# Kernel optimization log

Measured on AMD Instinct MI355X. Metric: run time of the kernel, lower is better.

The kernel has to match this reference:

```python
import jax, jax.numpy as jnp
import numpy as np

D_MODEL = 1024
NHEAD = 16
HEAD_DIM = D_MODEL // NHEAD
SF_THRESHOLD = 4.0
SF_LEVELS = 8
STEP = SF_THRESHOLD / SF_LEVELS  # quantization step of ScaleAndFireNeuron
EPS = 1e-6


def setup_inputs() -> dict:
    key = jax.random.key(0)
    ks = jax.random.split(key, 12)
    B, L, D = 2, 2048, D_MODEL
    s = 1.0 / np.sqrt(D)
    inp = {
        "x": jax.random.normal(ks[0], (B, L, D), dtype=jnp.float32),
        "wq": jax.random.normal(ks[1], (D, D), dtype=jnp.float32) * s,
        "bq": jnp.zeros((D,), dtype=jnp.float32),
        "wk": jax.random.normal(ks[2], (D, D), dtype=jnp.float32) * s,
        "bk": jnp.zeros((D,), dtype=jnp.float32),
        "wv": jax.random.normal(ks[3], (D, D), dtype=jnp.float32) * s,
        "bv": jnp.zeros((D,), dtype=jnp.float32),
        "wo": jax.random.normal(ks[4], (D, D), dtype=jnp.float32) * s,
        "bo": jnp.zeros((D,), dtype=jnp.float32),
        "gq": jnp.ones((HEAD_DIM,), dtype=jnp.float32),  # SpikingQKNorm gain (q)
        "gk": jnp.ones((HEAD_DIM,), dtype=jnp.float32),  # SpikingQKNorm gain (k)
    }
    return inp


def _rms_norm(t, g):
    # SpikingQKNorm: RMS normalization over head_dim with learned gain
    return t * jax.lax.rsqrt(jnp.mean(t * t, axis=-1, keepdims=True) + EPS) * g


def _sfn(t):
    # ScaleAndFireNeuron: T=1 multi-level spike quantization with straight-through estimator.
    # Levels are integer multiples of STEP, clipped to +/- SF_LEVELS.
    q = jnp.clip(jnp.round(t / STEP), -SF_LEVELS, SF_LEVELS) * STEP
    return t + jax.lax.stop_gradient(q - t)


def reference(x, wq, bq, wk, bk, wv, bv, wo, bo, gq, gk):
    B, L, D = x.shape
    H, Dh = NHEAD, HEAD_DIM
    scale = Dh ** -0.5

    def proj(w, b):
        return (x @ w.T + b).reshape(B, L, H, Dh).transpose(0, 2, 1, 3)  # [B,H,L,Dh]

    q = _sfn(_rms_norm(proj(wq, bq), gq))
    k = _sfn(_rms_norm(proj(wk, bk), gk))
    v = _sfn(proj(wv, bv))

    scores = jnp.einsum('bhqd,bhkd->bhqk', q, k) * scale  # [B,H,L,L]
    probs = jax.nn.softmax(scores, axis=-1)
    out = jnp.einsum('bhqk,bhkd->bhqd', probs, v)  # [B,H,L,Dh]
    out = out.transpose(0, 2, 1, 3).reshape(B, L, D)
    return out @ wo.T + bo
```

## Files before the change

### kernel.cpp

```cpp
#include <hip/hip_runtime.h>
#include <stdint.h>

#define D_MODEL 1024
#define NHEAD 16
#define HEAD_DIM 64
#define SEQ 2048
#define BATCH 2
#define MROWS (BATCH*SEQ)
#define KVBLK 128
#define KVTILES (SEQ/KVBLK)

typedef unsigned short u16;
typedef short bf16x8 __attribute__((ext_vector_type(8)));
typedef float f32x4 __attribute__((ext_vector_type(4)));
typedef float f32x16 __attribute__((ext_vector_type(16)));

__device__ inline float bf2f(u16 h){ return __uint_as_float(((unsigned)h)<<16); }
__device__ inline u16 f2bf(float x){
  unsigned u = __float_as_uint(x);
  unsigned r = (u + 0x7FFFu + ((u>>16)&1u)) >> 16;
  return (u16)r;
}

__device__ inline f32x4 mfma_bf16(bf16x8 a, bf16x8 b, f32x4 c){
  return __builtin_amdgcn_mfma_f32_16x16x32_bf16(a, b, c, 0, 0, 0);
}
__device__ inline f32x16 mfma32_bf16(bf16x8 a, bf16x8 b, f32x16 c){
  return __builtin_amdgcn_mfma_f32_32x32x16_bf16(a, b, c, 0, 0, 0);
}

__device__ inline void gld_lds16(const u16* g, u16* l){
  __builtin_amdgcn_global_load_lds(
      (const __attribute__((address_space(1))) void*)g,
      (__attribute__((address_space(3))) void*)l, 16, 0, 0);
}

__device__ inline int swz8(int row){ return (row ^ (row >> 3)) & 7; }

__device__ inline uint32_t pack_bf2(float p0, float p1){
  uint32_t u0 = __float_as_uint(p0) + 0x8000u;
  uint32_t u1 = __float_as_uint(p1) + 0x8000u;
  return __builtin_amdgcn_perm(u1, u0, 0x07060302u);
}

__global__ __launch_bounds__(256) void pack_split(const float* __restrict__ src,
                                                  u16* __restrict__ hi, u16* __restrict__ lo, int n4){
  int i = blockIdx.x*256 + threadIdx.x;
  if (i >= n4) return;
  float4 v = ((const float4*)src)[i];
  float vv[4] = {v.x, v.y, v.z, v.w};
  u16 h[4], l[4];
  #pragma unroll
  for (int j=0;j<4;j++){
    h[j] = f2bf(vv[j]);
    l[j] = f2bf(vv[j] - bf2f(h[j]));
  }
  ((ushort4*)hi)[i] = make_ushort4(h[0],h[1],h[2],h[3]);
  ((ushort4*)lo)[i] = make_ushort4(l[0],l[1],l[2],l[3]);
}

__global__ __launch_bounds__(256) void pack_w(const float* __restrict__ wq, const float* __restrict__ wk,
                                              const float* __restrict__ wv, const float* __restrict__ wo,
                                              u16* __restrict__ qkv_hi, u16* __restrict__ qkv_lo,
                                              u16* __restrict__ wo_hi, u16* __restrict__ wo_lo){
  int which = blockIdx.x >> 10;
  int i = ((blockIdx.x & 1023) << 8) + threadIdx.x;
  const float* src = which==0 ? wq : which==1 ? wk : which==2 ? wv : wo;
  u16* hi = (which==3) ? wo_hi : qkv_hi + ((size_t)which << 20);
  u16* lo = (which==3) ? wo_lo : qkv_lo + ((size_t)which << 20);
  float4 v = ((const float4*)src)[i];
  float vv[4] = {v.x, v.y, v.z, v.w};
  u16 h[4], l[4];
  #pragma unroll
  for (int j=0;j<4;j++){
    h[j] = f2bf(vv[j]);
    l[j] = f2bf(vv[j] - bf2f(h[j]));
  }
  ((ushort4*)hi)[i] = make_ushort4(h[0],h[1],h[2],h[3]);
  ((ushort4*)lo)[i] = make_ushort4(l[0],l[1],l[2],l[3]);
}

__global__ __launch_bounds__(256) void pack_bias(const float* __restrict__ bq, const float* __restrict__ bk,
                                                 const float* __restrict__ bv, float* __restrict__ out){
  int i = blockIdx.x*256 + threadIdx.x;
  if (i < 1024) out[i] = bq[i];
  else if (i < 2048) out[i] = bk[i-1024];
  else if (i < 3072) out[i] = bv[i-2048];
}

__global__ __launch_bounds__(256) void gemm_qkv(
    const u16* __restrict__ a_hi, const u16* __restrict__ a_lo,
    const u16* __restrict__ b_hi, const u16* __restrict__ b_lo,
    const float* __restrict__ bias,
    u16* __restrict__ qb, u16* __restrict__ kb, u16* __restrict__ vb,
    const float* __restrict__ gq, const float* __restrict__ gk)
{
  __shared__ u16 lds[2][12288];
  const int tid = threadIdx.x;
  const int lane = tid & 63;
  const int w = tid >> 6;
  const int wr = w >> 1, wc = w & 1;
  const int m0 = blockIdx.x * 128;
  const int n0 = blockIdx.y * 128;
  const int K = 1024;

  f32x4 acc[4][4];
  #pragma unroll
  for (int i=0;i<4;i++)
    #pragma unroll
    for (int j=0;j<4;j++) acc[i][j] = (f32x4){0.f,0.f,0.f,0.f};

  auto stage = [&](int buf, int kt){
    u16* base = &lds[buf][0];
    if (kt < 32){
      int kk = kt << 5;
      #pragma unroll
      for (int r=0;r<2;r++){
        const u16* g = a_hi + (size_t)(m0 + (tid>>2) + r*64)*K + kk + (tid&3)*8;
        gld_lds16(g, base + w*512 + r*2048);
      }
      #pragma unroll
      for (int r=0;r<2;r++){
        const u16* g = a_lo + (size_t)(m0 + (tid>>2) + r*64)*K + kk + (tid&3)*8;
        gld_lds16(g, base + 4096 + w*512 + r*2048);
      }
      #pragma unroll
      for (int r=0;r<2;r++){
        const u16* g = b_hi + (size_t)(n0 + (tid>>2) + r*64)*K + kk + (tid&3)*8;
        gld_lds16(g, base + 8192 + w*512 + r*2048);
      }
    } else {
      int kk = (kt-32) << 5;
      #pragma unroll
      for (int r=0;r<2;r++){
        const u16* g = a_hi + (size_t)(m0 + (tid>>2) + r*64)*K + kk + (tid&3)*8;
        gld_lds16(g, base + w*512 + r*2048);
      }
      #pragma unroll
      for (int r=0;r<2;r++){
        const u16* g = b_lo + (size_t)(n0 + (tid>>2) + r*64)*K + kk + (tid&3)*8;
        gld_lds16(g, base + 8192 + w*512 + r*2048);
      }
    }
  };

  const int koff = (lane>>4)*8;
  const int rowa = wr*64 + (lane&15);
  const int rowb = wc*64 + (lane&15);

  stage(0, 0);
  for (int kt=0; kt<64; ++kt){
    __syncthreads();
    if (kt+1 < 64) stage((kt+1)&1, kt+1);
    const u16* la = &lds[kt&1][0];
    const u16* lb = &lds[kt&1][8192];
    bf16x8 bfv[4];
    #pragma unroll
    for (int j=0;j<4;j++) bfv[j] = *(const bf16x8*)&lb[(rowb + j*16)*32 + koff];
    bf16x8 af[4];
    #pragma unroll
    for (int i=0;i<4;i++) af[i] = *(const bf16x8*)&la[(rowa + i*16)*32 + koff];
    #pragma unroll
    for (int i=0;i<4;i++)
      #pragma unroll
      for (int j=0;j<4;j++)
        acc[i][j] = mfma_bf16(af[i], bfv[j], acc[i][j]);
    if (kt < 32){
      const u16* ll = &lds[kt&1][4096];
      bf16x8 al[4];
      #pragma unroll
      for (int i=0;i<4;i++) al[i] = *(const bf16x8*)&ll[(rowa + i*16)*32 + koff];
      #pragma unroll
      for (int i=0;i<4;i++)
        #pragma unroll
        for (int j=0;j<4;j++)
          acc[i][j] = mfma_bf16(al[i], bfv[j], acc[i][j]);
    }
  }

  const int gcolbase = n0 + wc*64;
  const int sidx = gcolbase >> 6;
  const int ttype = sidx < 16 ? 0 : (sidx < 32 ? 1 : 2);
  u16* dst = ttype==0 ? qb : (ttype==1 ? kb : vb);
  const int h = sidx - (ttype==1 ? 16 : (ttype==2 ? 32 : 0));
  float gvals[4], bvals[4];
  #pragma unroll
  for (int j=0;j<4;j++){
    int dh = j*16 + (lane&15);
    bvals[j] = bias[gcolbase + dh];
    gvals[j] = ttype==0 ? gq[dh] : (ttype==1 ? gk[dh] : 1.0f);
  }
  #pragma unroll
  for (int i=0;i<4;i++){
    #pragma unroll
    for (int r=0;r<4;r++){
      float tv[4];
      float ssq = 0.f;
      #pragma unroll
      for (int j=0;j<4;j++){ tv[j] = acc[i][j][r] + bvals[j]; ssq += tv[j]*tv[j]; }
      ssq += __shfl_xor(ssq, 1);
      ssq += __shfl_xor(ssq, 2);
      ssq += __shfl_xor(ssq, 4);
      ssq += __shfl_xor(ssq, 8);
      float s = 1.0f;
      if (ttype < 2) s = 1.0f / sqrtf(ssq * (1.0f/64.0f) + 1e-6f);
      int row = m0 + wr*64 + i*16 + (lane>>4)*4 + r;
      int bi = row >> 11, li = row & 2047;
      size_t obase = ((size_t)(bi*NHEAD + h)*SEQ + li)*HEAD_DIM;
      #pragma unroll
      for (int j=0;j<4;j++){
        float val = tv[j] * s * gvals[j];
        float z = rintf(val * 2.0f);
        z = fminf(8.0f, fmaxf(-8.0f, z));
        dst[obase + j*16 + (lane&15)] = f2bf(z * 0.5f);
      }
    }
  }
}

__global__ __launch_bounds__(256) void gemm_bt(
    const u16* __restrict__ a_hi, const u16* __restrict__ b_hi,
    const float* __restrict__ bias, float* __restrict__ out_f,
    int M, int N, int K)
{
  __shared__ u16 lds[2][8192];
  const int tid = threadIdx.x;
  const int lane = tid & 63;
  const int w = tid >> 6;
  const int wr = w >> 1, wc = w & 1;
  const int m0 = blockIdx.x * 128;
  const int n0 = blockIdx.y * 128;
  const int NT = K / 32;

  f32x4 acc[4][4];
  #pragma unroll
  for (int i=0;i<4;i++)
    #pragma unroll
    for (int j=0;j<4;j++) acc[i][j] = (f32x4){0.f,0.f,0.f,0.f};

  auto stage = [&](int buf, int kt){
    int kk = kt * 32;
    u16* base = &lds[buf][0];
    #pragma unroll
    for (int r=0;r<2;r++){
      const u16* g = a_hi + (size_t)(m0 + (tid>>2) + r*64)*K + kk + (tid&3)*8;
      gld_lds16(g, base + w*512 + r*2048);
    }
    #pragma unroll
    for (int r=0;r<2;r++){
      const u16* g = b_hi + (size_t)(n0 + (tid>>2) + r*64)*K + kk + (tid&3)*8;
      gld_lds16(g, base + 4096 + w*512 + r*2048);
    }
  };

  stage(0, 0);
  for (int kt=0; kt<NT; ++kt){
    __syncthreads();
    if (kt+1 < NT) stage((kt+1)&1, kt+1);
    const u16* la = &lds[kt&1][0];
    const u16* lb = &lds[kt&1][4096];
    const int koff = (lane>>4)*8;
    const int rowa = wr*64 + (lane&15);
    const int rowb = wc*64 + (lane&15);
    bf16x8 af[4], bfv[4];
    #pragma unroll
    for (int i=0;i<4;i++) af[i]  = *(const bf16x8*)&la[(rowa + i*16)*32 + koff];
    #pragma unroll
    for (int i=0;i<4;i++) bfv[i] = *(const bf16x8*)&lb[(rowb + i*16)*32 + koff];
    #pragma unroll
    for (int i=0;i<4;i++)
      #pragma unroll
      for (int j=0;j<4;j++)
        acc[i][j] = mfma_bf16(af[i], bfv[j], acc[i][j]);
  }

  const int gcolbase = n0 + wc*64;
  #pragma unroll
  for (int j=0;j<4;j++){
    float bj = bias[gcolbase + j*16 + (lane&15)];
    #pragma unroll
    for (int i=0;i<4;i++){
      int row = m0 + wr*64 + i*16 + (lane>>4)*4;
      #pragma unroll
      for (int r=0;r<4;r++)
        out_f[(size_t)(row+r)*N + gcolbase + j*16 + (lane&15)] = acc[i][j][r] + bj;
    }
  }
}

__global__ __launch_bounds__(256) void transpose_v(const u16* __restrict__ v, u16* __restrict__ vt){
  __shared__ u16 tl[64][66];
  int bh = blockIdx.x >> 5;
  int l0 = (blockIdx.x & 31) * 64;
  int tid = threadIdx.x;
  #pragma unroll
  for (int it=0; it<2; ++it){
    int idx = tid + it*256;
    int row = idx >> 3, g = idx & 7;
    bf16x8 d = *(const bf16x8*)(v + ((size_t)bh*SEQ + l0 + row)*64 + g*8);
    #pragma unroll
    for (int j=0;j<8;j++) tl[row][g*8+j] = (u16)d[j];
  }
  __syncthreads();
  #pragma unroll
  for (int it=0; it<2; ++it){
    int idx = tid + it*256;
    int dh = idx >> 3, g = idx & 7;
    u16 tmp[8];
    #pragma unroll
    for (int j=0;j<8;j++) tmp[j] = tl[g*8+j][dh];
    *(bf16x8*)(vt + ((size_t)bh*HEAD_DIM + dh)*SEQ + l0 + g*8) = *(const bf16x8*)tmp;
  }
}

__global__ __launch_bounds__(256) void attn_kernel(
    const u16* __restrict__ qb, const u16* __restrict__ kb, const u16* __restrict__ vt,
    u16* __restrict__ attn_out)
{
  __shared__ u16 lds_k[2][KVBLK*64];
  __shared__ u16 lds_v[2][64*KVBLK];
  const int tid = threadIdx.x, lane = tid & 63, w = tid >> 6;
  const int bh = blockIdx.y;
  const int q0 = blockIdx.x * 128;
  const size_t kvbase = (size_t)bh * SEQ * HEAD_DIM;
  const size_t vtbase = (size_t)bh * HEAD_DIM * SEQ;
  const int l31 = lane & 31, hi = lane >> 5;

  bf16x8 qf[4];
  #pragma unroll
  for (int kd=0; kd<4; kd++){
    const u16* g = qb + kvbase + (size_t)(q0 + w*32 + l31)*64 + kd*16 + hi*8;
    bf16x8 v = *(const bf16x8*)g;
    #pragma unroll
    for (int j=0;j<8;j++) ((u16*)&v)[j] = f2bf(bf2f((u16)v[j]) * 0.125f);
    qf[kd] = v;
  }

  float m_s = -3.0e38f, l_s = 0.f;
  f32x16 o0, o1;
  #pragma unroll
  for (int r=0;r<16;r++){ o0[r] = 0.f; o1[r] = 0.f; }

  auto stage = [&](int buf, int t){
    const int kv0 = t * KVBLK;
    #pragma unroll
    for (int r=0;r<4;r++){
      int idx = tid + r*256;
      int row = idx >> 3, grp = idx & 7;
      const u16* g = kb + kvbase + (size_t)(kv0 + row)*64 + ((grp ^ swz8(row))<<3);
      gld_lds16(g, &lds_k[buf][idx<<3]);
    }
    #pragma unroll
    for (int r=0;r<4;r++){
      int idx = tid + r*256;
      int row = idx >> 4, grp = idx & 15;
      const u16* g = vt + vtbase + (size_t)row*SEQ + kv0 + ((grp ^ swz8(row))<<3);
      gld_lds16(g, &lds_v[buf][idx<<3]);
    }
  };

  stage(0, 0);
  for (int t=0; t<KVTILES; ++t){
    __syncthreads();
    if (t+1 < KVTILES) stage((t+1)&1, t+1);
    const int buf = t & 1;

    #pragma unroll
    for (int half=0; half<2; ++half){
      f32x16 s0, s1;
      #pragma unroll
      for (int r=0;r<16;r++){ s0[r] = 0.f; s1[r] = 0.f; }
      const int row0 = half*64 + l31;
      const int row1 = half*64 + 32 + l31;
      __builtin_amdgcn_s_setprio(1);
      #pragma unroll
      for (int kd=0; kd<4; kd++){
        bf16x8 a0 = *(const bf16x8*)&lds_k[buf][row0*64 + (((kd*2+hi) ^ swz8(row0))<<3)];
        bf16x8 a1 = *(const bf16x8*)&lds_k[buf][row1*64 + (((kd*2+hi) ^ swz8(row1))<<3)];
        s0 = mfma32_bf16(a0, qf[kd], s0);
        s1 = mfma32_bf16(a1, qf[kd], s1);
      }
      __builtin_amdgcn_s_setprio(0);

      float pmax = s0[0];
      #pragma unroll
      for (int r=1;r<16;r++) pmax = fmaxf(pmax, s0[r]);
      #pragma unroll
      for (int r=0;r<16;r++) pmax = fmaxf(pmax, s1[r]);
      pmax = fmaxf(pmax, __shfl_xor(pmax, 32));

      if (__any(pmax - m_s > 8.0f)) {
        float mnew = fmaxf(m_s, pmax);
        float c = __expf(m_s - mnew);
        m_s = mnew;
        l_s *= c;
        #pragma unroll
        for (int r=0;r<16;r++){
          float cr = __shfl(c, (r&3) + 8*(r>>2) + 4*hi);
          o0[r] *= cr; o1[r] *= cr;
        }
      }

      float rsum = 0.f;
      #pragma unroll
      for (int r=0;r<16;r++){ float p = __expf(s0[r] - m_s); s0[r] = p; rsum += p; }
      #pragma unroll
      for (int r=0;r<16;r++){ float p = __expf(s1[r] - m_s); s1[r] = p; rsum += p; }
      rsum += __shfl_xor(rsum, 32);
      l_s += rsum;

      uint32_t W[2][4][2];
      #pragma unroll
      for (int g=0; g<4; g++){
        W[0][g][0] = pack_bf2(s0[g*4+0], s0[g*4+1]);
        W[0][g][1] = pack_bf2(s0[g*4+2], s0[g*4+3]);
        W[1][g][0] = pack_bf2(s1[g*4+0], s1[g*4+1]);
        W[1][g][1] = pack_bf2(s1[g*4+2], s1[g*4+3]);
      }
      bf16x8 pa[4];
      #pragma unroll
      for (int ks=0; ks<4; ks++){
        const int kvb = ks >> 1, ks0 = ks & 1;
        uint32_t own0 = hi ? W[kvb][ks0*2+1][0] : W[kvb][ks0*2][0];
        uint32_t own1 = hi ? W[kvb][ks0*2+1][1] : W[kvb][ks0*2][1];
        uint32_t t0   = hi ? W[kvb][ks0*2][0]   : W[kvb][ks0*2+1][0];
        uint32_t t1   = hi ? W[kvb][ks0*2][1]   : W[kvb][ks0*2+1][1];
        uint32_t sw0  = (uint32_t)__shfl_xor((int)t0, 32);
        uint32_t sw1  = (uint32_t)__shfl_xor((int)t1, 32);
        uint32_t words[4];
        words[0] = hi ? sw0 : own0;
        words[1] = hi ? sw1 : own1;
        words[2] = hi ? own0 : sw0;
        words[3] = hi ? own1 : sw1;
        pa[ks] = *(const bf16x8*)words;
      }

      __builtin_amdgcn_s_setprio(1);
      #pragma unroll
      for (int ks=0; ks<4; ks++){
        const int rv0 = l31, rv1 = 32 + l31;
        const int cg = half*8 + ks*2 + hi;
        bf16x8 vb0 = *(const bf16x8*)&lds_v[buf][rv0*KVBLK + ((cg ^ swz8(rv0))<<3)];
        bf16x8 vb1 = *(const bf16x8*)&lds_v[buf][rv1*KVBLK + ((cg ^ swz8(rv1))<<3)];
        o0 = mfma32_bf16(pa[ks], vb0, o0);
        o1 = mfma32_bf16(pa[ks], vb1, o1);
      }
      __builtin_amdgcn_s_setprio(0);
    }
  }

  const int b = bh >> 4, h = bh & 15;
  #pragma unroll
  for (int r=0;r<16;r++){
    int q = (r&3) + 8*(r>>2) + 4*hi;
    float linv = 1.0f / __shfl(l_s, q);
    int row = q0 + w*32 + q;
    size_t obase = ((size_t)b*SEQ + row)*D_MODEL + h*64;
    attn_out[obase + l31]      = f2bf(o0[r] * linv);
    attn_out[obase + 32 + l31] = f2bf(o1[r] * linv);
  }
}

extern "C" void kernel_launch(void* const* d_in, const int* in_sizes, int n_in,
                              void* d_out, int out_size, void* d_ws, size_t ws_size,
                              hipStream_t stream){
  const float* x  = (const float*)d_in[0];
  const float* wq = (const float*)d_in[1];
  const float* bq = (const float*)d_in[2];
  const float* wk = (const float*)d_in[3];
  const float* bk = (const float*)d_in[4];
  const float* wv = (const float*)d_in[5];
  const float* bv = (const float*)d_in[6];
  const float* wo = (const float*)d_in[7];
  const float* bo = (const float*)d_in[8];
  const float* gq = (const float*)d_in[9];
  const float* gk = (const float*)d_in[10];
  float* out = (float*)d_out;

  char* ws = (char*)d_ws;
  size_t off = 0;
  auto alloc = [&](size_t bytes) -> char* {
    char* p = ws + off; off += (bytes + 255) & ~(size_t)255; return p;
  };
  const size_t ND = (size_t)MROWS * D_MODEL;
  u16* x_hi    = (u16*)alloc(ND*2);
  u16* x_lo    = (u16*)alloc(ND*2);
  u16* wqkv_hi = (u16*)alloc((size_t)3072*1024*2);
  u16* wqkv_lo = (u16*)alloc((size_t)3072*1024*2);
  u16* wo_hi   = (u16*)alloc((size_t)1024*1024*2);
  u16* wo_lo   = (u16*)alloc((size_t)1024*1024*2);
  float* bqkv  = (float*)alloc(3072*4);
  u16* q_bf    = (u16*)alloc(ND*2);
  u16* k_bf    = (u16*)alloc(ND*2);
  u16* v_bf    = (u16*)alloc(ND*2);
  u16* vT      = (u16*)alloc(ND*2);
  u16* attn_bf = (u16*)alloc(ND*2);
  (void)ws_size; (void)in_sizes; (void)n_in; (void)out_size;

  pack_split<<<4096, 256, 0, stream>>>(x, x_hi, x_lo, (int)(ND/4));
  pack_w<<<4096, 256, 0, stream>>>(wq, wk, wv, wo, wqkv_hi, wqkv_lo, wo_hi, wo_lo);
  pack_bias<<<12, 256, 0, stream>>>(bq, bk, bv, bqkv);

  gemm_qkv<<<dim3(32,24), 256, 0, stream>>>(x_hi, x_lo, wqkv_hi, wqkv_lo, bqkv,
        q_bf, k_bf, v_bf, gq, gk);

  transpose_v<<<1024, 256, 0, stream>>>(v_bf, vT);

  attn_kernel<<<dim3(16,32), 256, 0, stream>>>(q_bf, k_bf, vT, attn_bf);

  gemm_bt<<<dim3(32,8), 256, 0, stream>>>(attn_bf, wo_hi, bo, out, MROWS, 1024, 1024);
}
```

Before: 181.4 us.

## Enlarge QKV GEMM tile to 256x256 with 4-stage swizzled LDS pipeline

Rewrites the QKV projection GEMM to use 512-thread blocks computing 256x256 tiles. It uses a 4-buffer LDS ring with two tiles prefetched, an XOR-swizzled LDS layout to avoid bank conflicts, and explicit vmcnt waits with raw barriers and setprio around the MFMA block. The split-precision hi/lo passes become a uniform 96-step loop. The separate bias-packing kernel is removed and biases are read directly. The grid drops to 192 blocks, which may underfill the 256 CUs, and 128 KB of LDS per block limits occupancy.

Result: no change. 183.9 us (+1.4%).

```diff
diff --git a/kernel.cpp b/kernel.cpp
--- a/kernel.cpp
+++ b/kernel.cpp
@@ -80,101 +80,79 @@
   ((ushort4*)lo)[i] = make_ushort4(l[0],l[1],l[2],l[3]);
 }
 
-__global__ __launch_bounds__(256) void pack_bias(const float* __restrict__ bq, const float* __restrict__ bk,
-                                                 const float* __restrict__ bv, float* __restrict__ out){
-  int i = blockIdx.x*256 + threadIdx.x;
-  if (i < 1024) out[i] = bq[i];
-  else if (i < 2048) out[i] = bk[i-1024];
-  else if (i < 3072) out[i] = bv[i-2048];
-}
-
-__global__ __launch_bounds__(256) void gemm_qkv(
+__global__ __launch_bounds__(512) void gemm_qkv(
     const u16* __restrict__ a_hi, const u16* __restrict__ a_lo,
     const u16* __restrict__ b_hi, const u16* __restrict__ b_lo,
-    const float* __restrict__ bias,
+    const float* __restrict__ bq, const float* __restrict__ bk_,
+    const float* __restrict__ bv,
     u16* __restrict__ qb, u16* __restrict__ kb, u16* __restrict__ vb,
     const float* __restrict__ gq, const float* __restrict__ gk)
 {
-  __shared__ u16 lds[2][12288];
+  __shared__ u16 ldsq[4][16384];
   const int tid = threadIdx.x;
   const int lane = tid & 63;
   const int w = tid >> 6;
-  const int wr = w >> 1, wc = w & 1;
-  const int m0 = blockIdx.x * 128;
-  const int n0 = blockIdx.y * 128;
-  const int K = 1024;
-
-  f32x4 acc[4][4];
-  #pragma unroll
-  for (int i=0;i<4;i++)
+  const int wr = w >> 2, wc = w & 3;
+  const int l15 = lane & 15;
+  const int m0 = blockIdx.x * 256;
+  const int n0 = blockIdx.y * 256;
+  const int NT = 96;
+
+  f32x4 acc[8][4];
+  #pragma unroll
+  for (int i=0;i<8;i++)
     #pragma unroll
     for (int j=0;j<4;j++) acc[i][j] = (f32x4){0.f,0.f,0.f,0.f};
 
-  auto stage = [&](int buf, int kt){
-    u16* base = &lds[buf][0];
-    if (kt < 32){
-      int kk = kt << 5;
-      #pragma unroll
-      for (int r=0;r<2;r++){
-        const u16* g = a_hi + (size_t)(m0 + (tid>>2) + r*64)*K + kk + (tid&3)*8;
-        gld_lds16(g, base + w*512 + r*2048);
-      }
-      #pragma unroll
-      for (int r=0;r<2;r++){
-        const u16* g = a_lo + (size_t)(m0 + (tid>>2) + r*64)*K + kk + (tid&3)*8;
-        gld_lds16(g, base + 4096 + w*512 + r*2048);
-      }
-      #pragma unroll
-      for (int r=0;r<2;r++){
-        const u16* g = b_hi + (size_t)(n0 + (tid>>2) + r*64)*K + kk + (tid&3)*8;
-        gld_lds16(g, base + 8192 + w*512 + r*2048);
-      }
-    } else {
-      int kk = (kt-32) << 5;
-      #pragma unroll
-      for (int r=0;r<2;r++){
-        const u16* g = a_hi + (size_t)(m0 + (tid>>2) + r*64)*K + kk + (tid&3)*8;
-        gld_lds16(g, base + w*512 + r*2048);
-      }
-      #pragma unroll
-      for (int r=0;r<2;r++){
-        const u16* g = b_lo + (size_t)(n0 + (tid>>2) + r*64)*K + kk + (tid&3)*8;
-        gld_lds16(g, base + 8192 + w*512 + r*2048);
-      }
+  auto stageq = [&](int t){
+    u16* base = &ldsq[t & 3][0];
+    const u16* As = ((t>>5)==1) ? a_lo : a_hi;
+    const u16* Bs = ((t>>5)==2) ? b_lo : b_hi;
+    const int kk = (t & 31) << 5;
+    #pragma unroll
+    for (int r2=0;r2<2;r2++){
+      int idx = tid + r2*512;
+      int row = idx >> 2, s = idx & 3;
+      int g = s ^ ((row >> 1) & 3);
+      gld_lds16(As + (size_t)(m0+row)*1024 + kk + (g<<3), base + (idx<<3));
+    }
+    #pragma unroll
+    for (int r2=0;r2<2;r2++){
+      int idx = tid + r2*512;
+      int row = idx >> 2, s = idx & 3;
+      int g = s ^ ((row >> 1) & 3);
+      gld_lds16(Bs + (size_t)(n0+row)*1024 + kk + (g<<3), base + 8192 + (idx<<3));
     }
   };
 
-  const int koff = (lane>>4)*8;
-  const int rowa = wr*64 + (lane&15);
-  const int rowb = wc*64 + (lane&15);
-
-  stage(0, 0);
-  for (int kt=0; kt<64; ++kt){
-    __syncthreads();
-    if (kt+1 < 64) stage((kt+1)&1, kt+1);
-    const u16* la = &lds[kt&1][0];
-    const u16* lb = &lds[kt&1][8192];
-    bf16x8 bfv[4];
-    #pragma unroll
-    for (int j=0;j<4;j++) bfv[j] = *(const bf16x8*)&lb[(rowb + j*16)*32 + koff];
-    bf16x8 af[4];
-    #pragma unroll
-    for (int i=0;i<4;i++) af[i] = *(const bf16x8*)&la[(rowa + i*16)*32 + koff];
-    #pragma unroll
-    for (int i=0;i<4;i++)
-      #pragma unroll
-      for (int j=0;j<4;j++)
-        acc[i][j] = mfma_bf16(af[i], bfv[j], acc[i][j]);
-    if (kt < 32){
-      const u16* ll = &lds[kt&1][4096];
-      bf16x8 al[4];
-      #pragma unroll
-      for (int i=0;i<4;i++) al[i] = *(const bf16x8*)&ll[(rowa + i*16)*32 + koff];
-      #pragma unroll
-      for (int i=0;i<4;i++)
-        #pragma unroll
-        for (int j=0;j<4;j++)
-          acc[i][j] = mfma_bf16(al[i], bfv[j], acc[i][j]);
+  const int slot = ((lane >> 4) ^ ((l15 >> 1) & 3)) << 3;
+
+  stageq(0); stageq(1);
+  asm volatile("s_waitcnt vmcnt(4)" ::: "memory");
+  __builtin_amdgcn_s_barrier();
+
+  for (int t=0; t<NT; ++t){
+    if (t+2 < NT) stageq(t+2);
+    const u16* la = &ldsq[t & 3][0];
+    const u16* lb = &ldsq[t & 3][8192];
+    bf16x8 af[8], bfr[4];
+    #pragma unroll
+    for (int mf=0;mf<8;mf++)
+      af[mf] = *(const bf16x8*)&la[(wr*128 + mf*16 + l15)*32 + slot];
+    #pragma unroll
+    for (int nf=0;nf<4;nf++)
+      bfr[nf] = *(const bf16x8*)&lb[(wc*64 + nf*16 + l15)*32 + slot];
+    __builtin_amdgcn_s_setprio(1);
+    #pragma unroll
+    for (int mf=0;mf<8;mf++)
+      #pragma unroll
+      for (int nf=0;nf<4;nf++)
+        acc[mf][nf] = mfma_bf16(af[mf], bfr[nf], acc[mf][nf]);
+    __builtin_amdgcn_s_setprio(0);
+    if (t+1 < NT){
+      if (t+2 < NT) asm volatile("s_waitcnt vmcnt(4)" ::: "memory");
+      else          asm volatile("s_waitcnt vmcnt(0)" ::: "memory");
+      __builtin_amdgcn_s_barrier();
     }
   }
 
@@ -182,29 +160,30 @@
   const int sidx = gcolbase >> 6;
   const int ttype = sidx < 16 ? 0 : (sidx < 32 ? 1 : 2);
   u16* dst = ttype==0 ? qb : (ttype==1 ? kb : vb);
+  const float* bsrc = ttype==0 ? bq : (ttype==1 ? bk_ : bv);
   const int h = sidx - (ttype==1 ? 16 : (ttype==2 ? 32 : 0));
   float gvals[4], bvals[4];
   #pragma unroll
   for (int j=0;j<4;j++){
-    int dh = j*16 + (lane&15);
-    bvals[j] = bias[gcolbase + dh];
+    int dh = j*16 + l15;
+    bvals[j] = bsrc[(gcolbase & 1023) + dh];
     gvals[j] = ttype==0 ? gq[dh] : (ttype==1 ? gk[dh] : 1.0f);
   }
   #pragma unroll
-  for (int i=0;i<4;i++){
+  for (int mf=0;mf<8;mf++){
     #pragma unroll
     for (int r=0;r<4;r++){
       float tv[4];
       float ssq = 0.f;
       #pragma unroll
-      for (int j=0;j<4;j++){ tv[j] = acc[i][j][r] + bvals[j]; ssq += tv[j]*tv[j]; }
+      for (int j=0;j<4;j++){ tv[j] = acc[mf][j][r] + bvals[j]; ssq += tv[j]*tv[j]; }
       ssq += __shfl_xor(ssq, 1);
       ssq += __shfl_xor(ssq, 2);
       ssq += __shfl_xor(ssq, 4);
       ssq += __shfl_xor(ssq, 8);
       float s = 1.0f;
       if (ttype < 2) s = 1.0f / sqrtf(ssq * (1.0f/64.0f) + 1e-6f);
-      int row = m0 + wr*64 + i*16 + (lane>>4)*4 + r;
+      int row = m0 + wr*128 + mf*16 + (lane>>4)*4 + r;
       int bi = row >> 11, li = row & 2047;
       size_t obase = ((size_t)(bi*NHEAD + h)*SEQ + li)*HEAD_DIM;
       #pragma unroll
@@ -212,7 +191,7 @@
         float val = tv[j] * s * gvals[j];
         float z = rintf(val * 2.0f);
         z = fminf(8.0f, fmaxf(-8.0f, z));
-        dst[obase + j*16 + (lane&15)] = f2bf(z * 0.5f);
+        dst[obase + j*16 + l15] = f2bf(z * 0.5f);
       }
     }
   }
@@ -489,7 +468,6 @@
   u16* wqkv_lo = (u16*)alloc((size_t)3072*1024*2);
   u16* wo_hi   = (u16*)alloc((size_t)1024*1024*2);
   u16* wo_lo   = (u16*)alloc((size_t)1024*1024*2);
-  float* bqkv  = (float*)alloc(3072*4);
   u16* q_bf    = (u16*)alloc(ND*2);
   u16* k_bf    = (u16*)alloc(ND*2);
   u16* v_bf    = (u16*)alloc(ND*2);
@@ -499,10 +477,9 @@
 
   pack_split<<<4096, 256, 0, stream>>>(x, x_hi, x_lo, (int)(ND/4));
   pack_w<<<4096, 256, 0, stream>>>(wq, wk, wv, wo, wqkv_hi, wqkv_lo, wo_hi, wo_lo);
-  pack_bias<<<12, 256, 0, stream>>>(bq, bk, bv, bqkv);
-
-  gemm_qkv<<<dim3(32,24), 256, 0, stream>>>(x_hi, x_lo, wqkv_hi, wqkv_lo, bqkv,
-        q_bf, k_bf, v_bf, gq, gk);
+
+  gemm_qkv<<<dim3(16,12), 512, 0, stream>>>(x_hi, x_lo, wqkv_hi, wqkv_lo,
+        bq, bk, bv, q_bf, k_bf, v_bf, gq, gk);
 
   transpose_v<<<1024, 256, 0, stream>>>(v_bf, vT);
 
```
